# Kernel optimization log

Hardware: AMD Instinct MI355X
Metric: run time of the kernel (lower is better)

## Reference

```python
import jax, jax.numpy as jnp
import numpy as np

WEIGHT = 1e-7       # lambda for the CRF loss
SIGMA_RGB = 15.0    # color-similarity bandwidth
SIGMA_XY = 100.0    # spatial-proximity bandwidth
SCALE = 0.5         # scale_factor (sigma_xy is multiplied by it in forward)


def setup_inputs() -> dict:
    key = jax.random.key(0)
    k1, k2 = jax.random.split(key)
    images = jax.random.uniform(k1, (4, 3, 128, 128), jnp.float32) * 255.0  # [0,255] RGB
    logits = jax.random.normal(k2, (4, 4, 128, 128), jnp.float32)
    segmentations = jax.nn.softmax(logits, axis=1)  # softmaxed logits, N*K*H*W
    return {"images": images, "segmentations": segmentations}


def _crf_loss(images, segmentations):
    n, k, h, w = segmentations.shape
    # F.interpolate(images, scale_factor=0.5, mode='nearest') == stride-2 subsample
    img_s = images[:, :, ::2, ::2]
    # F.interpolate(segs, scale_factor=0.5, mode='bilinear', align_corners=False)
    # for exact /2 downscale == 2x2 average pooling
    hs, ws = h // 2, w // 2
    seg_s = segmentations.reshape(n, k, hs, 2, ws, 2).mean(axis=(3, 5))  # [n,k,hs,ws]

    P = hs * ws
    yy, xx = jnp.meshgrid(jnp.arange(hs, dtype=jnp.float32),
                          jnp.arange(ws, dtype=jnp.float32), indexing='ij')
    sigma_xy_eff = SIGMA_XY * SCALE
    pos = jnp.stack([xx, yy], axis=-1).reshape(P, 2) / sigma_xy_eff      # [P,2]
    rgb = img_s.reshape(n, 3, P).transpose(0, 2, 1) / SIGMA_RGB          # [n,P,3]
    feats = jnp.concatenate([jnp.broadcast_to(pos[None], (n, P, 2)), rgb], axis=-1)  # [n,P,5]

    # exact dense Gaussian bilateral kernel W_ij = exp(-0.5*||f_i - f_j||^2)
    sq = jnp.sum(feats * feats, axis=-1)                                 # [n,P]
    d2 = sq[:, :, None] + sq[:, None, :] - 2.0 * jnp.einsum('npc,nqc->npq', feats, feats)
    Wk = jnp.exp(-0.5 * jnp.maximum(d2, 0.0))                            # [n,P,P]

    S = seg_s.reshape(n, k, P)
    AS = jnp.einsum('npq,nkq->nkp', Wk, S)                               # bilateral-filtered segs
    loss = -jnp.sum(S * AS) / jnp.float32(n)
    return (WEIGHT * loss).reshape(1)


def reference(images, segmentations):
    return _crf_loss(images, segmentations)
```

## Files before the change

### kernel.cpp

```cpp
#include <hip/hip_runtime.h>

#define NB    4
#define PPB   4096
#define BLK   256
#define CHK   128
#define NCHK  32
#define NBLK3 528
#define NPART (NBLK3 * NB)

#if __has_builtin(__builtin_amdgcn_exp2f)
#define EXPFN(x) __builtin_amdgcn_exp2f(x)
#define FSCALE 1.2011224087864498f
#else
#define EXPFN(x) __expf(x)
#define FSCALE 1.0f
#endif

typedef __attribute__((ext_vector_type(8))) short short8v;
typedef __attribute__((ext_vector_type(4))) float f32x4;

typedef unsigned int uint;
typedef unsigned short ushort;

__device__ __forceinline__ ushort bsplit(float v, float& rem) {
    uint u = __float_as_uint(v);
    uint r = (u + 0x7FFFu + ((u >> 16) & 1u)) >> 16;
    rem = v - __uint_as_float(r << 16);
    return (ushort)r;
}

__global__ __launch_bounds__(256) void crf_prep(const float* __restrict__ images,
                                                const float* __restrict__ segs,
                                                uint* __restrict__ FA,
                                                uint* __restrict__ FB,
                                                uint* __restrict__ SA,
                                                uint* __restrict__ SB,
                                                float* __restrict__ H) {
    int gid = blockIdx.x * BLK + threadIdx.x;
    int n = gid >> 12;
    int p = gid & (PPB - 1);
    int i = p >> 6;
    int j = p & 63;
    int off = 256 * i + 2 * j;
    const float* img = images + (size_t)n * 3 * 16384;
    float f[5];
    f[0] = (float)j * (FSCALE / 50.0f);
    f[1] = (float)i * (FSCALE / 50.0f);
    f[2] = img[off]         * (FSCALE / 15.0f);
    f[3] = img[16384 + off] * (FSCALE / 15.0f);
    f[4] = img[32768 + off] * (FSCALE / 15.0f);
    float h = -0.5f * (f[0]*f[0] + f[1]*f[1] + f[2]*f[2] + f[3]*f[3] + f[4]*f[4]);

    const float* sg = segs + (size_t)n * 4 * 16384;
    float s[4];
#pragma unroll
    for (int k = 0; k < 4; ++k) {
        float2 u0 = *(const float2*)(sg + k * 16384 + off);
        float2 u1 = *(const float2*)(sg + k * 16384 + off + 128);
        s[k] = 0.25f * ((u0.x + u0.y) + (u1.x + u1.y));
    }

    ushort v[3][5];
    ushort tg[2][4];
#pragma unroll
    for (int c = 0; c < 5; ++c) {
        float r1, r2, dead;
        v[0][c] = bsplit(f[c], r1);
        v[1][c] = bsplit(r1, r2);
        v[2][c] = bsplit(r2, dead);
    }
#pragma unroll
    for (int c = 0; c < 4; ++c) {
        float r1, dead;
        tg[0][c] = bsplit(s[c], r1);
        tg[1][c] = bsplit(r1, dead);
    }

    static const int PA[6] = {0, 0, 1, 0, 1, 2};
    static const int PB[6] = {0, 1, 0, 2, 1, 0};
    uint fa[16], fb[16], sa[16], sb[16];
#pragma unroll
    for (int k2 = 0; k2 < 16; ++k2) {
        int s0 = 2 * k2, s1 = s0 + 1;
        uint lo = (s0 >= 30) ? 0u : (uint)v[PA[s0 / 5]][s0 % 5];
        uint hi = (s1 >= 30) ? 0u : (uint)v[PA[s1 / 5]][s1 % 5];
        fa[k2] = lo | (hi << 16);
        lo = (s0 >= 30) ? 0u : (uint)v[PB[s0 / 5]][s0 % 5];
        hi = (s1 >= 30) ? 0u : (uint)v[PB[s1 / 5]][s1 % 5];
        fb[k2] = lo | (hi << 16);
    }
    static const int QA[3] = {0, 0, 1};
    static const int QB[3] = {0, 1, 0};
#pragma unroll
    for (int k2 = 0; k2 < 16; ++k2) {
        int s0 = 2 * k2, s1 = s0 + 1;
        uint lo = (s0 >= 12) ? 0u : (uint)tg[QA[s0 / 4]][s0 % 4];
        uint hi = (s1 >= 12) ? 0u : (uint)tg[QA[s1 / 4]][s1 % 4];
        sa[k2] = lo | (hi << 16);
        lo = (s0 >= 12) ? 0u : (uint)tg[QB[s0 / 4]][s0 % 4];
        hi = (s1 >= 12) ? 0u : (uint)tg[QB[s1 / 4]][s1 % 4];
        sb[k2] = lo | (hi << 16);
    }

    uint4* fap = (uint4*)(FA + (size_t)gid * 16);
    uint4* fbp = (uint4*)(FB + (size_t)gid * 16);
    uint4* sap = (uint4*)(SA + (size_t)gid * 16);
    uint4* sbp = (uint4*)(SB + (size_t)gid * 16);
#pragma unroll
    for (int k = 0; k < 4; ++k) {
        fap[k] = make_uint4(fa[4*k], fa[4*k+1], fa[4*k+2], fa[4*k+3]);
        fbp[k] = make_uint4(fb[4*k], fb[4*k+1], fb[4*k+2], fb[4*k+3]);
        sap[k] = make_uint4(sa[4*k], sa[4*k+1], sa[4*k+2], sa[4*k+3]);
        sbp[k] = make_uint4(sb[4*k], sb[4*k+1], sb[4*k+2], sb[4*k+3]);
    }
    H[gid] = h;
}

__global__ __launch_bounds__(256, 4) void crf_pairs(const uint4* __restrict__ FA,
                                                    const uint4* __restrict__ FB,
                                                    const uint4* __restrict__ SA,
                                                    const uint4* __restrict__ SB,
                                                    const float* __restrict__ H,
                                                    float* __restrict__ part) {
    __shared__ float wsum[BLK / 64];
    int t = threadIdx.x;
    int n = blockIdx.y;
    int lane = t & 63;
    int w = t >> 6;
    int l15 = lane & 15;
    int lhi = lane >> 4;

    int b = blockIdx.x;
    int pc = 0;
#pragma unroll
    for (int i = 1; i < NCHK; ++i) pc += (b >= (i * (2 * NCHK + 1 - i)) / 2) ? 1 : 0;
    int qc = b - (pc * (2 * NCHK + 1 - pc)) / 2 + pc;
    bool diagblk = (pc == qc);
    int base = n << 12;
    int prow0 = pc * CHK + w * 32;

    size_t ar = (size_t)(base + prow0 + l15) * 4 + lhi;
    short8v a0  = __builtin_bit_cast(short8v, FA[ar]);
    short8v a1  = __builtin_bit_cast(short8v, FA[ar + 64]);
    short8v sa0 = __builtin_bit_cast(short8v, SA[ar]);
    short8v sa1 = __builtin_bit_cast(short8v, SA[ar + 64]);
    float hp0[4], hp1[4];
#pragma unroll
    for (int r = 0; r < 4; ++r) {
        hp0[r] = H[base + prow0 + lhi * 4 + r];
        hp1[r] = H[base + prow0 + 16 + lhi * 4 + r];
    }

    float accP = 0.f;
    float accD = 0.f;

#pragma unroll
    for (int jj = 0; jj < 8; ++jj) {
        if (diagblk && jj < 2 * w) continue;
        int qrow0 = qc * CHK + jj * 16;
        size_t br = (size_t)(base + qrow0 + l15) * 4 + lhi;
        short8v bf  = __builtin_bit_cast(short8v, FB[br]);
        short8v sbf = __builtin_bit_cast(short8v, SB[br]);
        float hq = H[base + qrow0 + l15];

        f32x4 cf0 = {0.f, 0.f, 0.f, 0.f};
        f32x4 cf1 = {0.f, 0.f, 0.f, 0.f};
        f32x4 cs0 = {0.f, 0.f, 0.f, 0.f};
        f32x4 cs1 = {0.f, 0.f, 0.f, 0.f};
        cf0 = __builtin_amdgcn_mfma_f32_16x16x32_bf16(a0, bf, cf0, 0, 0, 0);
        cf1 = __builtin_amdgcn_mfma_f32_16x16x32_bf16(a1, bf, cf1, 0, 0, 0);
        cs0 = __builtin_amdgcn_mfma_f32_16x16x32_bf16(sa0, sbf, cs0, 0, 0, 0);
        cs1 = __builtin_amdgcn_mfma_f32_16x16x32_bf16(sa1, sbf, cs1, 0, 0, 0);

        if (!diagblk) {
#pragma unroll
            for (int r = 0; r < 4; ++r) {
                accP = fmaf(EXPFN(cf0[r] + (hp0[r] + hq)), cs0[r], accP);
                accP = fmaf(EXPFN(cf1[r] + (hp1[r] + hq)), cs1[r], accP);
            }
        } else {
            int qgb = qrow0 + l15;
            int pgb = prow0 + lhi * 4;
#pragma unroll
            for (int r = 0; r < 4; ++r) {
                float w0 = EXPFN(cf0[r] + (hp0[r] + hq));
                int pg0 = pgb + r;
                float f0 = (qgb > pg0) ? 2.0f : ((qgb == pg0) ? 1.0f : 0.0f);
                accD = fmaf(w0 * f0, cs0[r], accD);
                float w1 = EXPFN(cf1[r] + (hp1[r] + hq));
                int pg1 = pg0 + 16;
                float f1 = (qgb > pg1) ? 2.0f : ((qgb == pg1) ? 1.0f : 0.0f);
                accD = fmaf(w1 * f1, cs1[r], accD);
            }
        }
    }

    float acc_all = 2.0f * accP + accD;
#pragma unroll
    for (int off = 32; off > 0; off >>= 1)
        acc_all += __shfl_down(acc_all, off, 64);
    if ((t & 63) == 0) wsum[t >> 6] = acc_all;
    __syncthreads();
    if (t == 0) {
        part[n * NBLK3 + blockIdx.x] =
            (wsum[0] + wsum[1]) + (wsum[2] + wsum[3]);
    }
}

__global__ __launch_bounds__(256) void crf_reduce(const float* __restrict__ part,
                                                  float* __restrict__ out) {
    __shared__ float wsum[BLK / 64];
    int t = threadIdx.x;
    float s = 0.f;
#pragma unroll
    for (int i = 0; i < 9; ++i) {
        int idx = t + i * BLK;
        if (idx < NPART) s += part[idx];
    }
#pragma unroll
    for (int off = 32; off > 0; off >>= 1)
        s += __shfl_down(s, off, 64);
    if ((t & 63) == 0) wsum[t >> 6] = s;
    __syncthreads();
    if (t == 0) {
        float tot = (wsum[0] + wsum[1]) + (wsum[2] + wsum[3]);
        out[0] = tot * (-2.5e-8f);
    }
}

extern "C" void kernel_launch(void* const* d_in, const int* in_sizes, int n_in,
                              void* d_out, int out_size, void* d_ws, size_t ws_size,
                              hipStream_t stream) {
    const float* images = (const float*)d_in[0];
    const float* segs   = (const float*)d_in[1];
    float* out = (float*)d_out;
    char* ws = (char*)d_ws;
    uint* FA = (uint*)(ws);
    uint* FB = (uint*)(ws + (1u << 20));
    uint* SA = (uint*)(ws + (2u << 20));
    uint* SB = (uint*)(ws + (3u << 20));
    float* H = (float*)(ws + (4u << 20));
    float* part = (float*)(ws + (4u << 20) + 65536);
    (void)in_sizes; (void)n_in; (void)out_size; (void)ws_size;

    crf_prep<<<dim3(64), dim3(256), 0, stream>>>(images, segs, FA, FB, SA, SB, H);
    crf_pairs<<<dim3(NBLK3, NB), dim3(256), 0, stream>>>(
        (const uint4*)FA, (const uint4*)FB, (const uint4*)SA, (const uint4*)SB, H, part);
    crf_reduce<<<dim3(1), dim3(256), 0, stream>>>(part, out);
}
```

Before: 80.41 us.

## Fuse prep, pair and reduce kernels into one with LDS staging and atomics

Folds the feature-preparation kernel into the pair kernel. Each block now recomputes its own 128 p-rows and 128 q-rows of split-bf16 features and segment weights and stages them in shared memory, instead of reading them from a global workspace. The final reduction kernel is replaced by a memset plus a per-block atomicAdd into the output. This removes two kernel launches and the global round trip, at the cost of redundant prep work in every block (each chunk is recomputed many times), an extra barrier, and a non-deterministic order of the atomic sum.

After: 88.75 us. 10.4% more time.

```diff
diff --git a/kernel.cpp b/kernel.cpp
--- a/kernel.cpp
+++ b/kernel.cpp
@@ -1,12 +1,10 @@
 #include <hip/hip_runtime.h>
 
 #define NB    4
-#define PPB   4096
 #define BLK   256
 #define CHK   128
 #define NCHK  32
 #define NBLK3 528
-#define NPART (NBLK3 * NB)
 
 #if __has_builtin(__builtin_amdgcn_exp2f)
 #define EXPFN(x) __builtin_amdgcn_exp2f(x)
@@ -29,100 +27,17 @@
     return (ushort)r;
 }
 
-__global__ __launch_bounds__(256) void crf_prep(const float* __restrict__ images,
-                                                const float* __restrict__ segs,
-                                                uint* __restrict__ FA,
-                                                uint* __restrict__ FB,
-                                                uint* __restrict__ SA,
-                                                uint* __restrict__ SB,
-                                                float* __restrict__ H) {
-    int gid = blockIdx.x * BLK + threadIdx.x;
-    int n = gid >> 12;
-    int p = gid & (PPB - 1);
-    int i = p >> 6;
-    int j = p & 63;
-    int off = 256 * i + 2 * j;
-    const float* img = images + (size_t)n * 3 * 16384;
-    float f[5];
-    f[0] = (float)j * (FSCALE / 50.0f);
-    f[1] = (float)i * (FSCALE / 50.0f);
-    f[2] = img[off]         * (FSCALE / 15.0f);
-    f[3] = img[16384 + off] * (FSCALE / 15.0f);
-    f[4] = img[32768 + off] * (FSCALE / 15.0f);
-    float h = -0.5f * (f[0]*f[0] + f[1]*f[1] + f[2]*f[2] + f[3]*f[3] + f[4]*f[4]);
-
-    const float* sg = segs + (size_t)n * 4 * 16384;
-    float s[4];
-#pragma unroll
-    for (int k = 0; k < 4; ++k) {
-        float2 u0 = *(const float2*)(sg + k * 16384 + off);
-        float2 u1 = *(const float2*)(sg + k * 16384 + off + 128);
-        s[k] = 0.25f * ((u0.x + u0.y) + (u1.x + u1.y));
-    }
-
-    ushort v[3][5];
-    ushort tg[2][4];
-#pragma unroll
-    for (int c = 0; c < 5; ++c) {
-        float r1, r2, dead;
-        v[0][c] = bsplit(f[c], r1);
-        v[1][c] = bsplit(r1, r2);
-        v[2][c] = bsplit(r2, dead);
-    }
-#pragma unroll
-    for (int c = 0; c < 4; ++c) {
-        float r1, dead;
-        tg[0][c] = bsplit(s[c], r1);
-        tg[1][c] = bsplit(r1, dead);
-    }
-
-    static const int PA[6] = {0, 0, 1, 0, 1, 2};
-    static const int PB[6] = {0, 1, 0, 2, 1, 0};
-    uint fa[16], fb[16], sa[16], sb[16];
-#pragma unroll
-    for (int k2 = 0; k2 < 16; ++k2) {
-        int s0 = 2 * k2, s1 = s0 + 1;
-        uint lo = (s0 >= 30) ? 0u : (uint)v[PA[s0 / 5]][s0 % 5];
-        uint hi = (s1 >= 30) ? 0u : (uint)v[PA[s1 / 5]][s1 % 5];
-        fa[k2] = lo | (hi << 16);
-        lo = (s0 >= 30) ? 0u : (uint)v[PB[s0 / 5]][s0 % 5];
-        hi = (s1 >= 30) ? 0u : (uint)v[PB[s1 / 5]][s1 % 5];
-        fb[k2] = lo | (hi << 16);
-    }
-    static const int QA[3] = {0, 0, 1};
-    static const int QB[3] = {0, 1, 0};
-#pragma unroll
-    for (int k2 = 0; k2 < 16; ++k2) {
-        int s0 = 2 * k2, s1 = s0 + 1;
-        uint lo = (s0 >= 12) ? 0u : (uint)tg[QA[s0 / 4]][s0 % 4];
-        uint hi = (s1 >= 12) ? 0u : (uint)tg[QA[s1 / 4]][s1 % 4];
-        sa[k2] = lo | (hi << 16);
-        lo = (s0 >= 12) ? 0u : (uint)tg[QB[s0 / 4]][s0 % 4];
-        hi = (s1 >= 12) ? 0u : (uint)tg[QB[s1 / 4]][s1 % 4];
-        sb[k2] = lo | (hi << 16);
-    }
-
-    uint4* fap = (uint4*)(FA + (size_t)gid * 16);
-    uint4* fbp = (uint4*)(FB + (size_t)gid * 16);
-    uint4* sap = (uint4*)(SA + (size_t)gid * 16);
-    uint4* sbp = (uint4*)(SB + (size_t)gid * 16);
-#pragma unroll
-    for (int k = 0; k < 4; ++k) {
-        fap[k] = make_uint4(fa[4*k], fa[4*k+1], fa[4*k+2], fa[4*k+3]);
-        fbp[k] = make_uint4(fb[4*k], fb[4*k+1], fb[4*k+2], fb[4*k+3]);
-        sap[k] = make_uint4(sa[4*k], sa[4*k+1], sa[4*k+2], sa[4*k+3]);
-        sbp[k] = make_uint4(sb[4*k], sb[4*k+1], sb[4*k+2], sb[4*k+3]);
-    }
-    H[gid] = h;
-}
-
-__global__ __launch_bounds__(256, 4) void crf_pairs(const uint4* __restrict__ FA,
-                                                    const uint4* __restrict__ FB,
-                                                    const uint4* __restrict__ SA,
-                                                    const uint4* __restrict__ SB,
-                                                    const float* __restrict__ H,
-                                                    float* __restrict__ part) {
+__global__ __launch_bounds__(256) void crf_fused(const float* __restrict__ images,
+                                                 const float* __restrict__ segs,
+                                                 float* __restrict__ out) {
+    __shared__ uint FAl[CHK][20];
+    __shared__ uint SAl[CHK][20];
+    __shared__ uint FBl[CHK][20];
+    __shared__ uint SBl[CHK][20];
+    __shared__ float Hp[CHK];
+    __shared__ float Hq[CHK];
     __shared__ float wsum[BLK / 64];
+
     int t = threadIdx.x;
     int n = blockIdx.y;
     int lane = t & 63;
@@ -136,19 +51,99 @@
     for (int i = 1; i < NCHK; ++i) pc += (b >= (i * (2 * NCHK + 1 - i)) / 2) ? 1 : 0;
     int qc = b - (pc * (2 * NCHK + 1 - pc)) / 2 + pc;
     bool diagblk = (pc == qc);
-    int base = n << 12;
-    int prow0 = pc * CHK + w * 32;
-
-    size_t ar = (size_t)(base + prow0 + l15) * 4 + lhi;
-    short8v a0  = __builtin_bit_cast(short8v, FA[ar]);
-    short8v a1  = __builtin_bit_cast(short8v, FA[ar + 64]);
-    short8v sa0 = __builtin_bit_cast(short8v, SA[ar]);
-    short8v sa1 = __builtin_bit_cast(short8v, SA[ar + 64]);
+
+    {
+        int side = t >> 7;
+        int r    = t & 127;
+        int p    = (side ? qc : pc) * CHK + r;
+        int i = p >> 6;
+        int j = p & 63;
+        int off = 256 * i + 2 * j;
+        const float* img = images + (size_t)n * 3 * 16384;
+        float f[5];
+        f[0] = (float)j * (FSCALE / 50.0f);
+        f[1] = (float)i * (FSCALE / 50.0f);
+        f[2] = img[off]         * (FSCALE / 15.0f);
+        f[3] = img[16384 + off] * (FSCALE / 15.0f);
+        f[4] = img[32768 + off] * (FSCALE / 15.0f);
+        float h = -0.5f * (f[0]*f[0] + f[1]*f[1] + f[2]*f[2] + f[3]*f[3] + f[4]*f[4]);
+
+        const float* sg = segs + (size_t)n * 4 * 16384;
+        float s[4];
+#pragma unroll
+        for (int k = 0; k < 4; ++k) {
+            float2 u0 = *(const float2*)(sg + k * 16384 + off);
+            float2 u1 = *(const float2*)(sg + k * 16384 + off + 128);
+            s[k] = 0.25f * ((u0.x + u0.y) + (u1.x + u1.y));
+        }
+
+        ushort v[3][5];
+        ushort tg[2][4];
+#pragma unroll
+        for (int c = 0; c < 5; ++c) {
+            float r1, r2, dead;
+            v[0][c] = bsplit(f[c], r1);
+            v[1][c] = bsplit(r1, r2);
+            v[2][c] = bsplit(r2, dead);
+        }
+#pragma unroll
+        for (int c = 0; c < 4; ++c) {
+            float r1, dead;
+            tg[0][c] = bsplit(s[c], r1);
+            tg[1][c] = bsplit(r1, dead);
+        }
+
+        uint fw[16], sw[16];
+        if (side == 0) {
+            static const int PA[6] = {0, 0, 1, 0, 1, 2};
+            static const int QA[3] = {0, 0, 1};
+#pragma unroll
+            for (int k2 = 0; k2 < 16; ++k2) {
+                int s0 = 2 * k2, s1 = s0 + 1;
+                uint lo = (s0 >= 30) ? 0u : (uint)v[PA[s0 / 5]][s0 % 5];
+                uint hi = (s1 >= 30) ? 0u : (uint)v[PA[s1 / 5]][s1 % 5];
+                fw[k2] = lo | (hi << 16);
+                lo = (s0 >= 12) ? 0u : (uint)tg[QA[s0 / 4]][s0 % 4];
+                hi = (s1 >= 12) ? 0u : (uint)tg[QA[s1 / 4]][s1 % 4];
+                sw[k2] = lo | (hi << 16);
+            }
+        } else {
+            static const int PB[6] = {0, 1, 0, 2, 1, 0};
+            static const int QB[3] = {0, 1, 0};
+#pragma unroll
+            for (int k2 = 0; k2 < 16; ++k2) {
+                int s0 = 2 * k2, s1 = s0 + 1;
+                uint lo = (s0 >= 30) ? 0u : (uint)v[PB[s0 / 5]][s0 % 5];
+                uint hi = (s1 >= 30) ? 0u : (uint)v[PB[s1 / 5]][s1 % 5];
+                fw[k2] = lo | (hi << 16);
+                lo = (s0 >= 12) ? 0u : (uint)tg[QB[s0 / 4]][s0 % 4];
+                hi = (s1 >= 12) ? 0u : (uint)tg[QB[s1 / 4]][s1 % 4];
+                sw[k2] = lo | (hi << 16);
+            }
+        }
+
+        uint* fd = side ? FBl[r] : FAl[r];
+        uint* sd = side ? SBl[r] : SAl[r];
+#pragma unroll
+        for (int k = 0; k < 4; ++k) {
+            *(uint4*)&fd[4 * k] = make_uint4(fw[4*k], fw[4*k+1], fw[4*k+2], fw[4*k+3]);
+            *(uint4*)&sd[4 * k] = make_uint4(sw[4*k], sw[4*k+1], sw[4*k+2], sw[4*k+3]);
+        }
+        if (side) Hq[r] = h;
+        else      Hp[r] = h;
+    }
+    __syncthreads();
+
+    int prow0 = w * 32;
+    short8v a0  = __builtin_bit_cast(short8v, *(const uint4*)&FAl[prow0 + l15][lhi * 4]);
+    short8v a1  = __builtin_bit_cast(short8v, *(const uint4*)&FAl[prow0 + 16 + l15][lhi * 4]);
+    short8v sa0 = __builtin_bit_cast(short8v, *(const uint4*)&SAl[prow0 + l15][lhi * 4]);
+    short8v sa1 = __builtin_bit_cast(short8v, *(const uint4*)&SAl[prow0 + 16 + l15][lhi * 4]);
     float hp0[4], hp1[4];
 #pragma unroll
     for (int r = 0; r < 4; ++r) {
-        hp0[r] = H[base + prow0 + lhi * 4 + r];
-        hp1[r] = H[base + prow0 + 16 + lhi * 4 + r];
+        hp0[r] = Hp[prow0 + lhi * 4 + r];
+        hp1[r] = Hp[prow0 + 16 + lhi * 4 + r];
     }
 
     float accP = 0.f;
@@ -157,11 +152,10 @@
 #pragma unroll
     for (int jj = 0; jj < 8; ++jj) {
         if (diagblk && jj < 2 * w) continue;
-        int qrow0 = qc * CHK + jj * 16;
-        size_t br = (size_t)(base + qrow0 + l15) * 4 + lhi;
-        short8v bf  = __builtin_bit_cast(short8v, FB[br]);
-        short8v sbf = __builtin_bit_cast(short8v, SB[br]);
-        float hq = H[base + qrow0 + l15];
+        int qr = jj * 16;
+        short8v bf  = __builtin_bit_cast(short8v, *(const uint4*)&FBl[qr + l15][lhi * 4]);
+        short8v sbf = __builtin_bit_cast(short8v, *(const uint4*)&SBl[qr + l15][lhi * 4]);
+        float hq = Hq[qr + l15];
 
         f32x4 cf0 = {0.f, 0.f, 0.f, 0.f};
         f32x4 cf1 = {0.f, 0.f, 0.f, 0.f};
@@ -179,17 +173,17 @@
                 accP = fmaf(EXPFN(cf1[r] + (hp1[r] + hq)), cs1[r], accP);
             }
         } else {
-            int qgb = qrow0 + l15;
-            int pgb = prow0 + lhi * 4;
+            int ql = qr + l15;
+            int pl = prow0 + lhi * 4;
 #pragma unroll
             for (int r = 0; r < 4; ++r) {
                 float w0 = EXPFN(cf0[r] + (hp0[r] + hq));
-                int pg0 = pgb + r;
-                float f0 = (qgb > pg0) ? 2.0f : ((qgb == pg0) ? 1.0f : 0.0f);
+                int pg0 = pl + r;
+                float f0 = (ql > pg0) ? 2.0f : ((ql == pg0) ? 1.0f : 0.0f);
                 accD = fmaf(w0 * f0, cs0[r], accD);
                 float w1 = EXPFN(cf1[r] + (hp1[r] + hq));
                 int pg1 = pg0 + 16;
-                float f1 = (qgb > pg1) ? 2.0f : ((qgb == pg1) ? 1.0f : 0.0f);
+                float f1 = (ql > pg1) ? 2.0f : ((ql == pg1) ? 1.0f : 0.0f);
                 accD = fmaf(w1 * f1, cs1[r], accD);
             }
         }
@@ -202,29 +196,8 @@
     if ((t & 63) == 0) wsum[t >> 6] = acc_all;
     __syncthreads();
     if (t == 0) {
-        part[n * NBLK3 + blockIdx.x] =
-            (wsum[0] + wsum[1]) + (wsum[2] + wsum[3]);
-    }
-}
-
-__global__ __launch_bounds__(256) void crf_reduce(const float* __restrict__ part,
-                                                  float* __restrict__ out) {
-    __shared__ float wsum[BLK / 64];
-    int t = threadIdx.x;
-    float s = 0.f;
-#pragma unroll
-    for (int i = 0; i < 9; ++i) {
-        int idx = t + i * BLK;
-        if (idx < NPART) s += part[idx];
-    }
-#pragma unroll
-    for (int off = 32; off > 0; off >>= 1)
-        s += __shfl_down(s, off, 64);
-    if ((t & 63) == 0) wsum[t >> 6] = s;
-    __syncthreads();
-    if (t == 0) {
-        float tot = (wsum[0] + wsum[1]) + (wsum[2] + wsum[3]);
-        out[0] = tot * (-2.5e-8f);
+        float s = (wsum[0] + wsum[1]) + (wsum[2] + wsum[3]);
+        atomicAdd(out, s * (-2.5e-8f));
     }
 }
 
@@ -234,17 +207,8 @@
     const float* images = (const float*)d_in[0];
     const float* segs   = (const float*)d_in[1];
     float* out = (float*)d_out;
-    char* ws = (char*)d_ws;
-    uint* FA = (uint*)(ws);
-    uint* FB = (uint*)(ws + (1u << 20));
-    uint* SA = (uint*)(ws + (2u << 20));
-    uint* SB = (uint*)(ws + (3u << 20));
-    float* H = (float*)(ws + (4u << 20));
-    float* part = (float*)(ws + (4u << 20) + 65536);
-    (void)in_sizes; (void)n_in; (void)out_size; (void)ws_size;
-
-    crf_prep<<<dim3(64), dim3(256), 0, stream>>>(images, segs, FA, FB, SA, SB, H);
-    crf_pairs<<<dim3(NBLK3, NB), dim3(256), 0, stream>>>(
-        (const uint4*)FA, (const uint4*)FB, (const uint4*)SA, (const uint4*)SB, H, part);
-    crf_reduce<<<dim3(1), dim3(256), 0, stream>>>(part, out);
+    (void)d_ws; (void)ws_size; (void)in_sizes; (void)n_in; (void)out_size;
+
+    (void)hipMemsetAsync(out, 0, sizeof(float), stream);
+    crf_fused<<<dim3(NBLK3, NB), dim3(256), 0, stream>>>(images, segs, out);
 }
```

## Drop reduce kernel via atomicAdd, split MFMA halves, raise occupancy

Applied to the files above, without the earlier changes.

Removes the final reduction kernel: each pairs block atomically adds its scaled partial sum into the output, which the prep kernel now zeroes. The prep launch changes from 64 blocks of 256 threads to 256 blocks of 64 so it spreads across more CUs. In the pairs kernel the two MFMA halves are interleaved with their exp consumption to lower register pressure, and launch bounds request 6 waves per SIMD. Float atomics make the sum order nondeterministic, and about two thousand atomics hit a single address.

New measurement: 97.29 us. 1.21x slower.

```diff
diff --git a/kernel.cpp b/kernel.cpp
--- a/kernel.cpp
+++ b/kernel.cpp
@@ -6,7 +6,6 @@
 #define CHK   128
 #define NCHK  32
 #define NBLK3 528
-#define NPART (NBLK3 * NB)
 
 #if __has_builtin(__builtin_amdgcn_exp2f)
 #define EXPFN(x) __builtin_amdgcn_exp2f(x)
@@ -29,14 +28,16 @@
     return (ushort)r;
 }
 
-__global__ __launch_bounds__(256) void crf_prep(const float* __restrict__ images,
-                                                const float* __restrict__ segs,
-                                                uint* __restrict__ FA,
-                                                uint* __restrict__ FB,
-                                                uint* __restrict__ SA,
-                                                uint* __restrict__ SB,
-                                                float* __restrict__ H) {
-    int gid = blockIdx.x * BLK + threadIdx.x;
+__global__ __launch_bounds__(64) void crf_prep(const float* __restrict__ images,
+                                               const float* __restrict__ segs,
+                                               uint* __restrict__ FA,
+                                               uint* __restrict__ FB,
+                                               uint* __restrict__ SA,
+                                               uint* __restrict__ SB,
+                                               float* __restrict__ H,
+                                               float* __restrict__ out) {
+    int gid = blockIdx.x * 64 + threadIdx.x;
+    if (gid == 0) out[0] = 0.0f;
     int n = gid >> 12;
     int p = gid & (PPB - 1);
     int i = p >> 6;
@@ -116,12 +117,12 @@
     H[gid] = h;
 }
 
-__global__ __launch_bounds__(256, 4) void crf_pairs(const uint4* __restrict__ FA,
+__global__ __launch_bounds__(256, 6) void crf_pairs(const uint4* __restrict__ FA,
                                                     const uint4* __restrict__ FB,
                                                     const uint4* __restrict__ SA,
                                                     const uint4* __restrict__ SB,
                                                     const float* __restrict__ H,
-                                                    float* __restrict__ part) {
+                                                    float* __restrict__ out) {
     __shared__ float wsum[BLK / 64];
     int t = threadIdx.x;
     int n = blockIdx.y;
@@ -164,32 +165,43 @@
         float hq = H[base + qrow0 + l15];
 
         f32x4 cf0 = {0.f, 0.f, 0.f, 0.f};
-        f32x4 cf1 = {0.f, 0.f, 0.f, 0.f};
         f32x4 cs0 = {0.f, 0.f, 0.f, 0.f};
-        f32x4 cs1 = {0.f, 0.f, 0.f, 0.f};
         cf0 = __builtin_amdgcn_mfma_f32_16x16x32_bf16(a0, bf, cf0, 0, 0, 0);
-        cf1 = __builtin_amdgcn_mfma_f32_16x16x32_bf16(a1, bf, cf1, 0, 0, 0);
         cs0 = __builtin_amdgcn_mfma_f32_16x16x32_bf16(sa0, sbf, cs0, 0, 0, 0);
-        cs1 = __builtin_amdgcn_mfma_f32_16x16x32_bf16(sa1, sbf, cs1, 0, 0, 0);
 
         if (!diagblk) {
 #pragma unroll
-            for (int r = 0; r < 4; ++r) {
+            for (int r = 0; r < 4; ++r)
                 accP = fmaf(EXPFN(cf0[r] + (hp0[r] + hq)), cs0[r], accP);
-                accP = fmaf(EXPFN(cf1[r] + (hp1[r] + hq)), cs1[r], accP);
-            }
         } else {
-            int qgb = qrow0 + l15;
-            int pgb = prow0 + lhi * 4;
+            int ql = qrow0 + l15;
+            int pl = prow0 + lhi * 4;
 #pragma unroll
             for (int r = 0; r < 4; ++r) {
                 float w0 = EXPFN(cf0[r] + (hp0[r] + hq));
-                int pg0 = pgb + r;
-                float f0 = (qgb > pg0) ? 2.0f : ((qgb == pg0) ? 1.0f : 0.0f);
+                int pg0 = pl + r;
+                float f0 = (ql > pg0) ? 2.0f : ((ql == pg0) ? 1.0f : 0.0f);
                 accD = fmaf(w0 * f0, cs0[r], accD);
+            }
+        }
+
+        f32x4 cf1 = {0.f, 0.f, 0.f, 0.f};
+        f32x4 cs1 = {0.f, 0.f, 0.f, 0.f};
+        cf1 = __builtin_amdgcn_mfma_f32_16x16x32_bf16(a1, bf, cf1, 0, 0, 0);
+        cs1 = __builtin_amdgcn_mfma_f32_16x16x32_bf16(sa1, sbf, cs1, 0, 0, 0);
+
+        if (!diagblk) {
+#pragma unroll
+            for (int r = 0; r < 4; ++r)
+                accP = fmaf(EXPFN(cf1[r] + (hp1[r] + hq)), cs1[r], accP);
+        } else {
+            int ql = qrow0 + l15;
+            int pl = prow0 + lhi * 4 + 16;
+#pragma unroll
+            for (int r = 0; r < 4; ++r) {
                 float w1 = EXPFN(cf1[r] + (hp1[r] + hq));
-                int pg1 = pg0 + 16;
-                float f1 = (qgb > pg1) ? 2.0f : ((qgb == pg1) ? 1.0f : 0.0f);
+                int pg1 = pl + r;
+                float f1 = (ql > pg1) ? 2.0f : ((ql == pg1) ? 1.0f : 0.0f);
                 accD = fmaf(w1 * f1, cs1[r], accD);
             }
         }
@@ -202,29 +214,8 @@
     if ((t & 63) == 0) wsum[t >> 6] = acc_all;
     __syncthreads();
     if (t == 0) {
-        part[n * NBLK3 + blockIdx.x] =
-            (wsum[0] + wsum[1]) + (wsum[2] + wsum[3]);
-    }
-}
-
-__global__ __launch_bounds__(256) void crf_reduce(const float* __restrict__ part,
-                                                  float* __restrict__ out) {
-    __shared__ float wsum[BLK / 64];
-    int t = threadIdx.x;
-    float s = 0.f;
-#pragma unroll
-    for (int i = 0; i < 9; ++i) {
-        int idx = t + i * BLK;
-        if (idx < NPART) s += part[idx];
-    }
-#pragma unroll
-    for (int off = 32; off > 0; off >>= 1)
-        s += __shfl_down(s, off, 64);
-    if ((t & 63) == 0) wsum[t >> 6] = s;
-    __syncthreads();
-    if (t == 0) {
-        float tot = (wsum[0] + wsum[1]) + (wsum[2] + wsum[3]);
-        out[0] = tot * (-2.5e-8f);
+        float s = (wsum[0] + wsum[1]) + (wsum[2] + wsum[3]);
+        atomicAdd(out, s * (-2.5e-8f));
     }
 }
 
@@ -240,11 +231,9 @@
     uint* SA = (uint*)(ws + (2u << 20));
     uint* SB = (uint*)(ws + (3u << 20));
     float* H = (float*)(ws + (4u << 20));
-    float* part = (float*)(ws + (4u << 20) + 65536);
     (void)in_sizes; (void)n_in; (void)out_size; (void)ws_size;
 
-    crf_prep<<<dim3(64), dim3(256), 0, stream>>>(images, segs, FA, FB, SA, SB, H);
+    crf_prep<<<dim3(256), dim3(64), 0, stream>>>(images, segs, FA, FB, SA, SB, H, out);
     crf_pairs<<<dim3(NBLK3, NB), dim3(256), 0, stream>>>(
-        (const uint4*)FA, (const uint4*)FB, (const uint4*)SA, (const uint4*)SB, H, part);
-    crf_reduce<<<dim3(1), dim3(256), 0, stream>>>(part, out);
-}
+        (const uint4*)FA, (const uint4*)FB, (const uint4*)SA, (const uint4*)SB, H, out);
+}
```
